# Kernel tuning notes

Measured on AMD Instinct MI355X. Metric: run time of the kernel, lower is better.

Reference implementation:

```python
import jax, jax.numpy as jnp
import numpy as np
import math

D_MODEL = 1024
N_HEADS = 16
D_K = D_MODEL // N_HEADS
MAX_REL = 32


def setup_inputs() -> dict:
    key = jax.random.key(0)
    ks = jax.random.split(key, 8)
    B, S = 8, 1024
    x = jax.random.normal(ks[0], (B, S, D_MODEL), dtype=jnp.float32)
    scale = 1.0 / math.sqrt(D_MODEL)
    Wq = jax.random.normal(ks[1], (D_MODEL, D_MODEL), dtype=jnp.float32) * scale
    Wk = jax.random.normal(ks[2], (D_MODEL, D_MODEL), dtype=jnp.float32) * scale
    Wv = jax.random.normal(ks[3], (D_MODEL, D_MODEL), dtype=jnp.float32) * scale
    Wo = jax.random.normal(ks[4], (D_MODEL, D_MODEL), dtype=jnp.float32) * scale
    b_o = jnp.zeros((D_MODEL,), dtype=jnp.float32)
    rel_k_emb = jax.random.normal(ks[5], (2 * MAX_REL + 1, D_K), dtype=jnp.float32) * 0.02
    rel_v_emb = jax.random.normal(ks[6], (2 * MAX_REL + 1, D_K), dtype=jnp.float32) * 0.02
    return {"x": x, "Wq": Wq, "Wk": Wk, "Wv": Wv, "Wo": Wo, "b_o": b_o,
            "rel_k_emb": rel_k_emb, "rel_v_emb": rel_v_emb}


def reference(x, Wq, Wk, Wv, Wo, b_o, rel_k_emb, rel_v_emb):
    B, S, D = x.shape
    H, dk = N_HEADS, D_K
    inv_sqrt_dk = 1.0 / math.sqrt(dk)
    # projections (torch Linear: x @ W.T), split heads -> [B, S, H, dk]
    Q = (x @ Wq.T).reshape(B, S, H, dk)
    K = (x @ Wk.T).reshape(B, S, H, dk)
    V = (x @ Wv.T).reshape(B, S, H, dk)
    # relative position indices: clip(j - i, -M, M) + M  -> [S, S]
    pos = jnp.arange(S)
    rel_idx = jnp.clip(pos[None, :] - pos[:, None], -MAX_REL, MAX_REL) + MAX_REL
    rel_k = rel_k_emb[rel_idx]  # [S, S, dk]
    rel_v = rel_v_emb[rel_idx]  # [S, S, dk]
    # scores: content term + Shaw relative-key term, both scaled by 1/sqrt(dk)
    scores = jnp.einsum('bihd,bjhd->bhij', Q, K) * inv_sqrt_dk
    scores = scores + jnp.einsum('bihd,ijd->bhij', Q, rel_k) * inv_sqrt_dk
    attn = jax.nn.softmax(scores, axis=-1)  # [B, H, S, S]
    # context: attn @ V + Shaw relative-value term
    ctx = jnp.einsum('bhij,bjhd->bihd', attn, V)
    ctx = ctx + jnp.einsum('bhij,ijd->bihd', attn, rel_v)
    ctx = ctx.reshape(B, S, D)
    out = ctx @ Wo.T + b_o
    return out
```

## Files before the change

### kernel.cpp

```cpp
#include <hip/hip_runtime.h>
#include <hip/hip_bf16.h>
#include <stdint.h>

typedef __bf16 bf16;
typedef __bf16 bf16x8 __attribute__((ext_vector_type(8)));
typedef short s16x4 __attribute__((ext_vector_type(4)));
typedef float f32x4 __attribute__((ext_vector_type(4)));

#define DEVI __device__ __forceinline__

static constexpr int QREL_ST = 80;
static constexpr float SCL2 = 0.1803368801111244f;

DEVI void gload_lds16(const void* g, void* l) {
  __builtin_amdgcn_global_load_lds(
      (const __attribute__((address_space(1))) void*)g,
      (__attribute__((address_space(3))) void*)l, 16, 0, 0);
}

__global__ __launch_bounds__(256) void k_cvt(const float* __restrict__ s,
                                             bf16* __restrict__ d, int n4) {
  int i = blockIdx.x * 256 + threadIdx.x;
  if (i >= n4) return;
  float4 v = ((const float4*)s)[i];
  union { bf16 b[4]; ushort4 u; } pk;
  pk.b[0] = (bf16)v.x; pk.b[1] = (bf16)v.y;
  pk.b[2] = (bf16)v.z; pk.b[3] = (bf16)v.w;
  ((ushort4*)d)[i] = pk.u;
}

__global__ __launch_bounds__(256) void k_cvtw(const float* __restrict__ a,
                                              const float* __restrict__ b,
                                              const float* __restrict__ c,
                                              const float* __restrict__ e,
                                              bf16* __restrict__ d) {
  int z = blockIdx.y;
  const float* s = (z == 0) ? a : (z == 1) ? b : (z == 2) ? c : e;
  int i = blockIdx.x * 256 + threadIdx.x;
  float4 v = ((const float4*)s)[i];
  union { bf16 bb[4]; ushort4 u; } pk;
  pk.bb[0] = (bf16)v.x; pk.bb[1] = (bf16)v.y;
  pk.bb[2] = (bf16)v.z; pk.bb[3] = (bf16)v.w;
  ((ushort4*)(d + (size_t)z * 1048576))[i] = pk.u;
}

template <int MODE>
DEVI void gemm_core(const bf16* __restrict__ A, const bf16* __restrict__ W,
                    const float* __restrict__ bo, bf16* __restrict__ OutB,
                    float* __restrict__ OutF, int m0, int n0) {
  const int tid = threadIdx.x, wid = tid >> 6, lane = tid & 63;
  const int wr = wid >> 1, wc = wid & 1;
  __shared__ __attribute__((aligned(16))) bf16 As[128 * 32];
  __shared__ __attribute__((aligned(16))) bf16 Bs[128 * 32];
  f32x4 acc[4][4] = {};
  const int lrow = lane >> 2, lcol = (lane & 3) * 8;
  for (int k0 = 0; k0 < 1024; k0 += 32) {
    for (int c = wid; c < 8; c += 4) {
      gload_lds16(&A[(size_t)(m0 + c * 16 + lrow) * 1024 + k0 + lcol], &As[c * 512]);
      gload_lds16(&W[(size_t)(n0 + c * 16 + lrow) * 1024 + k0 + lcol], &Bs[c * 512]);
    }
    __syncthreads();
    bf16x8 af[4], bw[4];
#pragma unroll
    for (int f = 0; f < 4; ++f) {
      af[f] = *(const bf16x8*)&As[(wr * 64 + f * 16 + (lane & 15)) * 32 + (lane >> 4) * 8];
      bw[f] = *(const bf16x8*)&Bs[(wc * 64 + f * 16 + (lane & 15)) * 32 + (lane >> 4) * 8];
    }
#pragma unroll
    for (int fm = 0; fm < 4; ++fm)
#pragma unroll
      for (int fn = 0; fn < 4; ++fn)
        acc[fm][fn] = __builtin_amdgcn_mfma_f32_16x16x32_bf16(af[fm], bw[fn], acc[fm][fn], 0, 0, 0);
    __syncthreads();
  }
#pragma unroll
  for (int fm = 0; fm < 4; ++fm)
#pragma unroll
    for (int fn = 0; fn < 4; ++fn)
#pragma unroll
      for (int r = 0; r < 4; ++r) {
        int m = m0 + wr * 64 + fm * 16 + (lane >> 4) * 4 + r;
        int n = n0 + wc * 64 + fn * 16 + (lane & 15);
        if (MODE == 0) {
          size_t o = ((size_t)((m >> 10) * 16 + (n >> 6)) * 1024 + (m & 1023)) * 64 + (n & 63);
          OutB[o] = (bf16)acc[fm][fn][r];
        } else {
          OutF[(size_t)m * 1024 + n] = acc[fm][fn][r] + bo[n];
        }
      }
}

__global__ __launch_bounds__(256) void k_gemm_qkv(const bf16* __restrict__ A,
                                                  const bf16* __restrict__ Wb,
                                                  bf16* __restrict__ Qb,
                                                  bf16* __restrict__ Kb,
                                                  bf16* __restrict__ Vb) {
  const int z = blockIdx.z;
  const bf16* W = Wb + (size_t)z * 1024 * 1024;
  bf16* Out = (z == 0) ? Qb : ((z == 1) ? Kb : Vb);
  gemm_core<0>(A, W, nullptr, Out, nullptr, blockIdx.x * 128, blockIdx.y * 128);
}

__global__ __launch_bounds__(256) void k_gemm_out(const bf16* __restrict__ A,
                                                  const bf16* __restrict__ W,
                                                  const float* __restrict__ bo,
                                                  float* __restrict__ Out) {
  gemm_core<1>(A, W, bo, nullptr, Out, blockIdx.x * 128, blockIdx.y * 128);
}

__global__ __launch_bounds__(256) void k_transpose(const bf16* __restrict__ Vb,
                                                   bf16* __restrict__ Vt) {
  const int s0 = blockIdx.x * 64, bh = blockIdx.y;
  __shared__ __attribute__((aligned(16))) bf16 T[64 * 72];
  const int tid = threadIdx.x;
#pragma unroll
  for (int c = 0; c < 2; ++c) {
    int flat = c * 256 + tid;
    int row = flat >> 3, c8 = (flat & 7) * 8;
    *(uint4*)&T[row * 72 + c8] =
        *(const uint4*)&Vb[((size_t)bh * 1024 + s0 + row) * 64 + c8];
  }
  __syncthreads();
  const int d = tid >> 2, j0 = (tid & 3) * 16;
  union { bf16 b[16]; uint4 u[2]; } pk;
#pragma unroll
  for (int j = 0; j < 16; ++j) pk.b[j] = T[(j0 + j) * 72 + d];
  size_t base = ((size_t)bh * 64 + d) * 1024 + s0 + j0;
  *(uint4*)&Vt[base] = pk.u[0];
  *(uint4*)&Vt[base + 8] = pk.u[1];
}

__global__ __launch_bounds__(256) void k_qrel(const bf16* __restrict__ Qb,
                                              const float* __restrict__ relk,
                                              bf16* __restrict__ Qrel) {
  const int m0 = blockIdx.x * 64;
  const int tid = threadIdx.x, wid = tid >> 6, lane = tid & 63;
  __shared__ __attribute__((aligned(16))) bf16 RK[80 * 72];
  for (int i = tid; i < 80 * 72; i += 256) {
    int r = i / 72, dd = i % 72;
    RK[i] = (r < 65 && dd < 64) ? (bf16)relk[r * 64 + dd] : (bf16)0.0f;
  }
  __syncthreads();
  bf16x8 qa[2];
#pragma unroll
  for (int kk = 0; kk < 2; ++kk)
    qa[kk] = *(const bf16x8*)&Qb[(size_t)(m0 + wid * 16 + (lane & 15)) * 64 + kk * 32 + (lane >> 4) * 8];
  f32x4 acc[5] = {};
#pragma unroll
  for (int fc = 0; fc < 5; ++fc)
#pragma unroll
    for (int kk = 0; kk < 2; ++kk) {
      bf16x8 rb = *(const bf16x8*)&RK[(fc * 16 + (lane & 15)) * 72 + kk * 32 + (lane >> 4) * 8];
      acc[fc] = __builtin_amdgcn_mfma_f32_16x16x32_bf16(qa[kk], rb, acc[fc], 0, 0, 0);
    }
#pragma unroll
  for (int fc = 0; fc < 5; ++fc)
#pragma unroll
    for (int r = 0; r < 4; ++r)
      Qrel[(size_t)(m0 + wid * 16 + (lane >> 4) * 4 + r) * QREL_ST + fc * 16 + (lane & 15)] =
          (bf16)(acc[fc][r] * SCL2);
}

__global__ __launch_bounds__(256) void k_prep(const float* __restrict__ relv,
                                              bf16* __restrict__ RVt) {
  int i = blockIdx.x * 256 + threadIdx.x;
  if (i >= 64 * 96) return;
  int d = i / 96, r = i % 96;
  RVt[i] = (r < 65) ? (bf16)relv[r * 64 + d] : (bf16)0.0f;
}

__global__ __launch_bounds__(256, 4) void k_attn(const bf16* __restrict__ Qb,
                                                 const bf16* __restrict__ Kb,
                                                 const bf16* __restrict__ Vt,
                                                 const bf16* __restrict__ Qrel,
                                                 const bf16* __restrict__ RVt,
                                                 const float* __restrict__ relv,
                                                 bf16* __restrict__ Ctx) {
  const int jb = blockIdx.x;
  const int xcd = jb & 7, rlin = jb >> 3;
  const int bh = xcd + 8 * (rlin >> 4);
  const int tq = rlin & 15, q0 = tq * 64;
  const int tid = threadIdx.x, wid = tid >> 6, lane = tid & 63;
  __shared__ __attribute__((aligned(16))) bf16 Qrl[64 * 72];
  __shared__ __attribute__((aligned(16))) bf16 KS[64 * 64];
  __shared__ __attribute__((aligned(16))) bf16 VS[64 * 64];
  __shared__ __attribute__((aligned(16))) bf16 BUK[64 * 64];

  for (int i = tid; i < 576; i += 256) {
    int row = i / 9, u4 = (i % 9) * 8;
    *(uint4*)&Qrl[row * 72 + u4] =
        *(const uint4*)&Qrel[((size_t)bh * 1024 + q0 + row) * QREL_ST + u4];
  }
  {
    uint4 z4 = {0, 0, 0, 0};
    uint4* bz = (uint4*)BUK;
    for (int i = tid; i < 512; i += 256) bz[i] = z4;
  }

  const int q16 = lane & 15, lhi = lane >> 4;
  const int qrow = wid * 16 + q16;
  const int qglob = q0 + qrow;
  const size_t kvb = (size_t)bh * 65536;

  const int srow = lane >> 3;
  const int scol = (((lane & 7) ^ srow)) * 8;

#define STAGE(T)                                                               \
  do {                                                                         \
    const int kv0_ = (T) * 64;                                                 \
    _Pragma("unroll")                                                          \
    for (int i = 0; i < 2; ++i) {                                              \
      const int c = wid * 2 + i;                                               \
      const int row = c * 8 + srow;                                            \
      gload_lds16(&Kb[kvb + (size_t)(kv0_ + row) * 64 + scol], &KS[c * 512]);  \
      gload_lds16(&Vt[kvb + (size_t)row * 1024 + kv0_ + scol], &VS[c * 512]);  \
    }                                                                          \
  } while (0)

  bf16x8 qa[2];
#pragma unroll
  for (int kk = 0; kk < 2; ++kk)
    qa[kk] = *(const bf16x8*)&Qb[kvb + (size_t)qglob * 64 + kk * 32 + lhi * 8];

  float biasL, biasR;

  f32x4 o[4] = {};
  float rowsum = 0.f, sumL = 0.f, sumR = 0.f;

  union PU { bf16 b[4]; s16x4 s; };
  union VU { uint2 u; s16x4 s; };

  STAGE(0);
  __syncthreads();
  biasL = (float)Qrl[qrow * 72 + 0];
  biasR = (float)Qrl[qrow * 72 + 64];

  const int swz = (q16 & 7) * 8;

  for (int t = 0; t < 16; ++t) {
    const int kv0 = t * 64;
    const int kind = (t <= tq - 2) ? 0 : (t >= tq + 2) ? 1 : 2;
    f32x4 st[4] = {};
#pragma unroll
    for (int jt = 0; jt < 4; ++jt)
#pragma unroll
      for (int kk = 0; kk < 2; ++kk) {
        bf16x8 kf = *(const bf16x8*)&KS[(jt * 16 + q16) * 64 + ((kk * 32 + lhi * 8) ^ swz)];
        st[jt] = __builtin_amdgcn_mfma_f32_16x16x32_bf16(kf, qa[kk], st[jt], 0, 0, 0);
      }
    PU pk[4];
    if (kind == 0) {
#pragma unroll
      for (int jt = 0; jt < 4; ++jt)
#pragma unroll
        for (int r = 0; r < 4; ++r) {
          float p = __builtin_amdgcn_exp2f(__builtin_fmaf(st[jt][r], SCL2, biasL));
          rowsum += p; sumL += p;
          pk[jt].b[r] = (bf16)p;
        }
    } else if (kind == 1) {
#pragma unroll
      for (int jt = 0; jt < 4; ++jt)
#pragma unroll
        for (int r = 0; r < 4; ++r) {
          float p = __builtin_amdgcn_exp2f(__builtin_fmaf(st[jt][r], SCL2, biasR));
          rowsum += p; sumR += p;
          pk[jt].b[r] = (bf16)p;
        }
    } else {
#pragma unroll
      for (int jt = 0; jt < 4; ++jt)
#pragma unroll
        for (int r = 0; r < 4; ++r) {
          const int j = kv0 + jt * 16 + lhi * 4 + r;
          const int delta = j - qglob;
          const int dc = delta < -32 ? -32 : (delta > 32 ? 32 : delta);
          const float b = (float)Qrl[qrow * 72 + dc + 32];
          float p = __builtin_amdgcn_exp2f(__builtin_fmaf(st[jt][r], SCL2, b));
          rowsum += p;
          pk[jt].b[r] = (bf16)p;
          if (delta <= -32) sumL += p;
          else if (delta >= 32) sumR += p;
          else BUK[qrow * 64 + delta + 32] = (bf16)p;
        }
    }
#pragma unroll
    for (int jt = 0; jt < 4; ++jt)
#pragma unroll
      for (int fd = 0; fd < 4; ++fd) {
        VU v;
        v.u = *(const uint2*)&VS[(fd * 16 + q16) * 64 + ((jt * 16 + lhi * 4) ^ swz)];
        o[fd] = __builtin_amdgcn_mfma_f32_16x16x16bf16_1k(pk[jt].s, v.s, o[fd], 0, 0, 0);
      }
    __syncthreads();
    if (t < 15) {
      STAGE(t + 1);
      __syncthreads();
    }
  }
#undef STAGE

  rowsum += __shfl_xor(rowsum, 16, 64);
  rowsum += __shfl_xor(rowsum, 32, 64);
  sumL += __shfl_xor(sumL, 16, 64);
  sumL += __shfl_xor(sumL, 32, 64);
  sumR += __shfl_xor(sumR, 16, 64);
  sumR += __shfl_xor(sumR, 32, 64);
  if (lhi == 0) BUK[qrow * 64 + 0] = (bf16)sumL;

  float linv[4], sumRr[4];
#pragma unroll
  for (int r = 0; r < 4; ++r) {
    linv[r] = 1.0f / __shfl(rowsum, lhi * 4 + r, 16);
    sumRr[r] = __shfl(sumR, lhi * 4 + r, 16);
  }

#pragma unroll
  for (int kk = 0; kk < 2; ++kk) {
    bf16x8 pa = *(const bf16x8*)&BUK[(wid * 16 + q16) * 64 + kk * 32 + lhi * 8];
#pragma unroll
    for (int fd = 0; fd < 4; ++fd) {
      bf16x8 rb = *(const bf16x8*)&RVt[(fd * 16 + q16) * 96 + kk * 32 + lhi * 8];
      o[fd] = __builtin_amdgcn_mfma_f32_16x16x32_bf16(pa, rb, o[fd], 0, 0, 0);
    }
  }
#pragma unroll
  for (int fd = 0; fd < 4; ++fd) {
    float rv64 = relv[64 * 64 + fd * 16 + q16];
#pragma unroll
    for (int r = 0; r < 4; ++r) o[fd][r] += sumRr[r] * rv64;
  }

  const int rbase = wid * 16 + lhi * 4;
  __syncthreads();
  bf16* OL = Qrl;
#pragma unroll
  for (int fd = 0; fd < 4; ++fd)
#pragma unroll
    for (int r = 0; r < 4; ++r)
      OL[(rbase + r) * 72 + fd * 16 + q16] = (bf16)(o[fd][r] * linv[r]);
  __syncthreads();
  {
    int il = tid >> 2, d0 = (tid & 3) * 16;
    union { bf16 b[16]; uint4 u[2]; } pkk;
#pragma unroll
    for (int c = 0; c < 16; ++c) pkk.b[c] = OL[il * 72 + d0 + c];
    size_t base = ((size_t)(bh >> 4) * 1024 + q0 + il) * 1024 + (bh & 15) * 64 + d0;
    *(uint4*)&Ctx[base] = pkk.u[0];
    *(uint4*)&Ctx[base + 8] = pkk.u[1];
  }
}

extern "C" void kernel_launch(void* const* d_in, const int* in_sizes, int n_in,
                              void* d_out, int out_size, void* d_ws, size_t ws_size,
                              hipStream_t stream) {
  const float* x = (const float*)d_in[0];
  const float* Wq = (const float*)d_in[1];
  const float* Wk = (const float*)d_in[2];
  const float* Wv = (const float*)d_in[3];
  const float* Wo = (const float*)d_in[4];
  const float* bo = (const float*)d_in[5];
  const float* relk = (const float*)d_in[6];
  const float* relv = (const float*)d_in[7];
  float* out = (float*)d_out;

  uint8_t* w = (uint8_t*)d_ws;
  bf16* xb = (bf16*)(w);
  bf16* Wb = (bf16*)(w + 16777216);
  bf16* Qb = (bf16*)(w + 25165824);
  bf16* Kb = (bf16*)(w + 41943040);
  bf16* Vb = (bf16*)(w + 58720256);
  bf16* Vt = (bf16*)(w + 75497472);
  bf16* Qrel = (bf16*)(w + 92274688);
  bf16* Ctx = Vb;
  bf16* RVt = xb;

  k_cvt<<<8192, 256, 0, stream>>>(x, xb, 2097152);
  k_cvtw<<<dim3(1024, 4), 256, 0, stream>>>(Wq, Wk, Wv, Wo, Wb);

  dim3 gg(64, 8, 3);
  k_gemm_qkv<<<gg, 256, 0, stream>>>(xb, Wb, Qb, Kb, Vb);
  k_transpose<<<dim3(16, 128), 256, 0, stream>>>(Vb, Vt);
  k_qrel<<<2048, 256, 0, stream>>>(Qb, relk, Qrel);
  k_prep<<<24, 256, 0, stream>>>(relv, RVt);
  k_attn<<<2048, 256, 0, stream>>>(Qb, Kb, Vt, Qrel, RVt, relv, Ctx);
  k_gemm_out<<<dim3(64, 8), 256, 0, stream>>>(Ctx, Wb + 3 * 1048576, bo, out);
}
```

Before: 201.3 us.

## Double-buffer K/V tiles and compute row sums via ones-column MFMA

K and V LDS tiles become double-buffered, so the next tile's async global-to-LDS load is issued at the start of each iteration and one of the two barriers per iteration goes away. Per-element scalar row-sum accumulation is replaced by an extra MFMA against a ones matrix, and the right-side sum is recovered by snapshotting that accumulator at the band boundary. This reduces VALU work and sync stalls in the softmax loop. In exchange it uses more LDS, so the occupancy hint drops from 4 to 3 blocks, and the row sums now come from bf16-rounded probabilities.

Result: slower. 214.7 us (+6.7%).

```diff
diff --git a/kernel.cpp b/kernel.cpp
--- a/kernel.cpp
+++ b/kernel.cpp
@@ -169,7 +169,7 @@
   RVt[i] = (r < 65) ? (bf16)relv[r * 64 + d] : (bf16)0.0f;
 }
 
-__global__ __launch_bounds__(256, 4) void k_attn(const bf16* __restrict__ Qb,
+__global__ __launch_bounds__(256, 3) void k_attn(const bf16* __restrict__ Qb,
                                                  const bf16* __restrict__ Kb,
                                                  const bf16* __restrict__ Vt,
                                                  const bf16* __restrict__ Qrel,
@@ -182,8 +182,9 @@
   const int tq = rlin & 15, q0 = tq * 64;
   const int tid = threadIdx.x, wid = tid >> 6, lane = tid & 63;
   __shared__ __attribute__((aligned(16))) bf16 Qrl[64 * 72];
-  __shared__ __attribute__((aligned(16))) bf16 KS[64 * 64];
-  __shared__ __attribute__((aligned(16))) bf16 VS[64 * 64];
+  __shared__ __attribute__((aligned(16))) bf16 KS[2][64 * 64];
+  __shared__ __attribute__((aligned(16))) bf16 VS[2][64 * 64];
+  __shared__ __attribute__((aligned(16))) bf16 ONES[16 * 64];
   __shared__ __attribute__((aligned(16))) bf16 BUK[64 * 64];
 
   for (int i = tid; i < 576; i += 256) {
@@ -196,6 +197,8 @@
     uint4* bz = (uint4*)BUK;
     for (int i = tid; i < 512; i += 256) bz[i] = z4;
   }
+  for (int i = tid; i < 1024; i += 256)
+    ONES[i] = (i < 64) ? (bf16)1.0f : (bf16)0.0f;
 
   const int q16 = lane & 15, lhi = lane >> 4;
   const int qrow = wid * 16 + q16;
@@ -205,15 +208,15 @@
   const int srow = lane >> 3;
   const int scol = (((lane & 7) ^ srow)) * 8;
 
-#define STAGE(T)                                                               \
+#define STAGE(T, KD, VD)                                                       \
   do {                                                                         \
     const int kv0_ = (T) * 64;                                                 \
     _Pragma("unroll")                                                          \
     for (int i = 0; i < 2; ++i) {                                              \
       const int c = wid * 2 + i;                                               \
       const int row = c * 8 + srow;                                            \
-      gload_lds16(&Kb[kvb + (size_t)(kv0_ + row) * 64 + scol], &KS[c * 512]);  \
-      gload_lds16(&Vt[kvb + (size_t)row * 1024 + kv0_ + scol], &VS[c * 512]);  \
+      gload_lds16(&Kb[kvb + (size_t)(kv0_ + row) * 64 + scol], &(KD)[c * 512]);\
+      gload_lds16(&Vt[kvb + (size_t)row * 1024 + kv0_ + scol], &(VD)[c * 512]);\
     }                                                                          \
   } while (0)
 
@@ -222,30 +225,33 @@
   for (int kk = 0; kk < 2; ++kk)
     qa[kk] = *(const bf16x8*)&Qb[kvb + (size_t)qglob * 64 + kk * 32 + lhi * 8];
 
-  float biasL, biasR;
-
   f32x4 o[4] = {};
-  float rowsum = 0.f, sumL = 0.f, sumR = 0.f;
+  f32x4 o4 = {};
+  f32x4 snapB = {};
+  float sumL = 0.f, sumR = 0.f;
 
   union PU { bf16 b[4]; s16x4 s; };
   union VU { uint2 u; s16x4 s; };
 
-  STAGE(0);
-  __syncthreads();
-  biasL = (float)Qrl[qrow * 72 + 0];
-  biasR = (float)Qrl[qrow * 72 + 64];
+  STAGE(0, KS[0], VS[0]);
+  __syncthreads();
+  const float biasL = (float)Qrl[qrow * 72 + 0];
+  const float biasR = (float)Qrl[qrow * 72 + 64];
 
   const int swz = (q16 & 7) * 8;
 
   for (int t = 0; t < 16; ++t) {
     const int kv0 = t * 64;
+    const bf16* Kc = KS[t & 1];
+    const bf16* Vc = VS[t & 1];
+    if (t < 15) STAGE(t + 1, KS[(t + 1) & 1], VS[(t + 1) & 1]);
     const int kind = (t <= tq - 2) ? 0 : (t >= tq + 2) ? 1 : 2;
     f32x4 st[4] = {};
 #pragma unroll
     for (int jt = 0; jt < 4; ++jt)
 #pragma unroll
       for (int kk = 0; kk < 2; ++kk) {
-        bf16x8 kf = *(const bf16x8*)&KS[(jt * 16 + q16) * 64 + ((kk * 32 + lhi * 8) ^ swz)];
+        bf16x8 kf = *(const bf16x8*)&Kc[(jt * 16 + q16) * 64 + ((kk * 32 + lhi * 8) ^ swz)];
         st[jt] = __builtin_amdgcn_mfma_f32_16x16x32_bf16(kf, qa[kk], st[jt], 0, 0, 0);
       }
     PU pk[4];
@@ -255,7 +261,7 @@
 #pragma unroll
         for (int r = 0; r < 4; ++r) {
           float p = __builtin_amdgcn_exp2f(__builtin_fmaf(st[jt][r], SCL2, biasL));
-          rowsum += p; sumL += p;
+          sumL += p;
           pk[jt].b[r] = (bf16)p;
         }
     } else if (kind == 1) {
@@ -264,7 +270,6 @@
 #pragma unroll
         for (int r = 0; r < 4; ++r) {
           float p = __builtin_amdgcn_exp2f(__builtin_fmaf(st[jt][r], SCL2, biasR));
-          rowsum += p; sumR += p;
           pk[jt].b[r] = (bf16)p;
         }
     } else {
@@ -277,7 +282,6 @@
           const int dc = delta < -32 ? -32 : (delta > 32 ? 32 : delta);
           const float b = (float)Qrl[qrow * 72 + dc + 32];
           float p = __builtin_amdgcn_exp2f(__builtin_fmaf(st[jt][r], SCL2, b));
-          rowsum += p;
           pk[jt].b[r] = (bf16)p;
           if (delta <= -32) sumL += p;
           else if (delta >= 32) sumR += p;
@@ -285,23 +289,23 @@
         }
     }
 #pragma unroll
-    for (int jt = 0; jt < 4; ++jt)
+    for (int jt = 0; jt < 4; ++jt) {
 #pragma unroll
       for (int fd = 0; fd < 4; ++fd) {
         VU v;
-        v.u = *(const uint2*)&VS[(fd * 16 + q16) * 64 + ((jt * 16 + lhi * 4) ^ swz)];
+        v.u = *(const uint2*)&Vc[(fd * 16 + q16) * 64 + ((jt * 16 + lhi * 4) ^ swz)];
         o[fd] = __builtin_amdgcn_mfma_f32_16x16x16bf16_1k(pk[jt].s, v.s, o[fd], 0, 0, 0);
       }
+      VU w1;
+      w1.u = *(const uint2*)&ONES[q16 * 64 + ((jt * 16 + lhi * 4) ^ swz)];
+      o4 = __builtin_amdgcn_mfma_f32_16x16x16bf16_1k(pk[jt].s, w1.s, o4, 0, 0, 0);
+    }
+    if (t == tq + 1) snapB = o4;
     __syncthreads();
-    if (t < 15) {
-      STAGE(t + 1);
-      __syncthreads();
-    }
   }
 #undef STAGE
-
-  rowsum += __shfl_xor(rowsum, 16, 64);
-  rowsum += __shfl_xor(rowsum, 32, 64);
+  if (tq == 15) snapB = o4;
+
   sumL += __shfl_xor(sumL, 16, 64);
   sumL += __shfl_xor(sumL, 32, 64);
   sumR += __shfl_xor(sumR, 16, 64);
@@ -311,8 +315,10 @@
   float linv[4], sumRr[4];
 #pragma unroll
   for (int r = 0; r < 4; ++r) {
-    linv[r] = 1.0f / __shfl(rowsum, lhi * 4 + r, 16);
-    sumRr[r] = __shfl(sumR, lhi * 4 + r, 16);
+    float bandR = __shfl(sumR, lhi * 4 + r, 16);
+    float diff = o4[r] - snapB[r];
+    sumRr[r] = bandR + __shfl(diff, lane & 48, 64);
+    linv[r] = 1.0f / __shfl(o4[r], lane & 48, 64);
   }
 
 #pragma unroll
```
